# Kernel tuning notes

Measured on AMD Instinct MI355X. Metric: run time of the kernel, lower is better.

## Reference

```python
import jax, jax.numpy as jnp
import numpy as np

S = 2048          # sequence length (single prefill sequence)
HID = 4096        # hidden_size
NH, NKV, HD = 32, 8, 128   # q heads, kv heads, head_dim
THETA = 10000.0
SCALE = HD ** -0.5


def setup_inputs() -> dict:
    key = jax.random.key(0)
    k1, k2, k3 = jax.random.split(key, 3)
    hidden_states = jax.random.normal(k1, (S, HID), jnp.float32)
    positions = jnp.arange(S, dtype=jnp.int32)
    W_qkv = jax.random.normal(k2, (HID, (NH + 2 * NKV) * HD), jnp.float32) * 0.02
    W_o = jax.random.normal(k3, (NH * HD, HID), jnp.float32) * 0.02
    return {"hidden_states": hidden_states, "positions": positions,
            "W_qkv": W_qkv, "W_o": W_o}


def _rope(x, positions):
    # x: [T, H, HD]; neox-style RoPE (rotate halves, is_neox_style=True)
    half = HD // 2
    inv_freq = 1.0 / (THETA ** (jnp.arange(half, dtype=jnp.float32) / half))
    freqs = positions.astype(jnp.float32)[:, None] * inv_freq[None, :]  # [T, half]
    cos = jnp.cos(freqs)[:, None, :]
    sin = jnp.sin(freqs)[:, None, :]
    x1, x2 = x[..., :half], x[..., half:]
    return jnp.concatenate([x1 * cos - x2 * sin, x2 * cos + x1 * sin], axis=-1)


def reference(hidden_states, positions, W_qkv, W_o):
    # fused QKV projection then split (q_size = NH*HD, kv_size = NKV*HD)
    qkv = hidden_states @ W_qkv                      # [S, (NH+2*NKV)*HD]
    q, k, v = jnp.split(qkv, [NH * HD, NH * HD + NKV * HD], axis=1)
    q = _rope(q.reshape(S, NH, HD), positions)       # [S, NH, HD]
    k = _rope(k.reshape(S, NKV, HD), positions)      # [S, NKV, HD]
    v = v.reshape(S, NKV, HD)
    # GQA: broadcast kv heads to query heads
    rep = NH // NKV
    k = jnp.repeat(k, rep, axis=1)                   # [S, NH, HD]
    v = jnp.repeat(v, rep, axis=1)
    scores = jnp.einsum('qhd,khd->hqk', q, k) * SCALE  # [NH, S, S]
    causal = jnp.tril(jnp.ones((S, S), dtype=bool))
    scores = jnp.where(causal[None], scores, jnp.finfo(scores.dtype).min)
    attn = jax.nn.softmax(scores, axis=-1)
    out = jnp.einsum('hqk,khd->qhd', attn, v).reshape(S, NH * HD)
    return out @ W_o                                 # [S, HID]
```

## Files before the change

kernel.cpp:

```cpp
#include <hip/hip_runtime.h>
#include <math.h>
#include <stdint.h>

#define S_LEN 2048
#define HID 4096
#define NH 32
#define NKV 8
#define HD 128
#define QKV_N ((NH + 2*NKV) * HD)
#define NQK (NH + NKV)
static __device__ __constant__ const float SCALE_F = 0.08838834764831845f;

typedef __bf16 bf16x8 __attribute__((ext_vector_type(8)));
typedef __bf16 bf16x4 __attribute__((ext_vector_type(4)));
typedef float  f32x4  __attribute__((ext_vector_type(4)));
typedef uint32_t u32x4 __attribute__((ext_vector_type(4)));

#define GLD_LDS(gptr, lptr) \
  __builtin_amdgcn_global_load_lds( \
      (const __attribute__((address_space(1))) uint32_t*)(gptr), \
      (__attribute__((address_space(3))) uint32_t*)(lptr), 16, 0, 0)

__device__ __forceinline__ void tp64(const float* __restrict__ in, __bf16* __restrict__ out,
                                     int R, int C, int bx, int by, int tid, float* tile) {
  int lr = tid >> 4;
  int lc = (tid & 15) * 4;
  #pragma unroll
  for (int p = 0; p < 4; ++p) {
    int r = p * 16 + lr;
    const float4 v = *(const float4*)&in[(size_t)(by + r) * C + bx + lc];
    float* t = &tile[r * 65 + lc];
    t[0] = v.x; t[1] = v.y; t[2] = v.z; t[3] = v.w;
  }
  __syncthreads();
  int oc = tid >> 5;
  int orr = (tid & 31) * 2;
  #pragma unroll
  for (int p = 0; p < 8; ++p) {
    int c = p * 8 + oc;
    float v0 = tile[orr * 65 + c];
    float v1 = tile[(orr + 1) * 65 + c];
    __bf16 b2[2] = { (__bf16)v0, (__bf16)v1 };
    *(uint32_t*)&out[(size_t)(bx + c) * R + by + orr] = *(uint32_t*)b2;
  }
}

__global__ __launch_bounds__(256) void fused_prep_kernel(const float* __restrict__ hidden,
                                                         __bf16* __restrict__ hid_bf,
                                                         const float* __restrict__ Wqkv,
                                                         __bf16* __restrict__ wqkvT) {
  __shared__ float tile[64 * 65];
  const int b = blockIdx.x;
  const int tid = threadIdx.x;
  if (b < 2048) {
    const float4* in4 = (const float4*)hidden;
    int i = b * 256 + tid;
    #pragma unroll
    for (int k = 0; k < 4; ++k) {
      float4 v = in4[i + k * 524288];
      bf16x4 o = { (__bf16)v.x, (__bf16)v.y, (__bf16)v.z, (__bf16)v.w };
      *(bf16x4*)(hid_bf + (size_t)(i + k * 524288) * 4) = o;
    }
  } else {
    int id = b - 2048;
    int bx = (id % 96) * 64, by = (id / 96) * 64;
    tp64(Wqkv, wqkvT, HID, QKV_N, bx, by, tid, tile);
  }
}

__global__ __launch_bounds__(256) void fused_rope_tpv_kernel(const __bf16* __restrict__ qkv,
                                                             const int* __restrict__ pos,
                                                             __bf16* __restrict__ Qr,
                                                             __bf16* __restrict__ Kr,
                                                             __bf16* __restrict__ Vt) {
  __shared__ __bf16 tile[32][33];
  const int b = blockIdx.x;
  const int tid = threadIdx.x;
  if (b < 20480) {
    int idx = b * 256 + tid;
    int half = idx & 63;
    int t = idx >> 6;
    int hh = t % NQK;
    int s = t / NQK;
    if (s >= S_LEN) return;
    float p = (float)pos[s];
    float inv_freq = exp2f((float)half * -0.2076205059304601f);
    float ang = p * inv_freq;
    float cs = cosf(ang), sn = sinf(ang);
    const __bf16* src; __bf16* dst;
    if (hh < NH) {
      src = qkv + (size_t)s * QKV_N + (size_t)hh * HD;
      dst = Qr + ((size_t)s * NH + hh) * HD;
    } else {
      int kh = hh - NH;
      src = qkv + (size_t)s * QKV_N + (size_t)NH * HD + (size_t)kh * HD;
      dst = Kr + ((size_t)s * NKV + kh) * HD;
    }
    float x1 = (float)src[half], x2 = (float)src[half + 64];
    dst[half]      = (__bf16)(x1 * cs - x2 * sn);
    dst[half + 64] = (__bf16)(x2 * cs + x1 * sn);
  } else {
    int id = b - 20480;
    int sb = (id & 63) * 32;
    int db = ((id >> 6) & 3) * 32;
    int kvh = id >> 8;
    int tx = tid & 31, ty = tid >> 5;
    const __bf16* src = qkv + (size_t)(NH + NKV) * HD + (size_t)kvh * HD;
    for (int i = 0; i < 32; i += 8)
      tile[ty + i][tx] = src[(size_t)(sb + ty + i) * QKV_N + db + tx];
    __syncthreads();
    for (int i = 0; i < 32; i += 8)
      Vt[((size_t)kvh * HD + db + ty + i) * S_LEN + sb + tx] = tile[tx][ty + i];
  }
}

template <int BN, typename OutT>
__global__ __launch_bounds__(512, 2) void gemm_flat_kernel(const __bf16* __restrict__ A,
                                                           const __bf16* __restrict__ Bt,
                                                           OutT* __restrict__ C,
                                                           int M, int N, int K) {
  constexpr int NF = BN / 64;
  constexpr uint32_t ABUF = 8192u;
  constexpr uint32_t BBUF = (uint32_t)BN * 64u;
  __shared__ __align__(16) __bf16 sA[4 * 128 * 32];
  __shared__ __align__(16) __bf16 sB[4 * BN * 32];
  const int tid = threadIdx.x;
  const int lane = tid & 63;
  const int wave = tid >> 6;
  const int quad = lane >> 4;
  const int l16 = lane & 15;
  const int wm = (wave >> 2) * 64;
  const int wn = (wave & 3) * (BN / 4);

  const int nx = gridDim.x, ny = gridDim.y;
  const int nwg = nx * ny;
  int lin = blockIdx.y * nx + blockIdx.x;
  size_t bm, bn;
  if ((nwg & 7) == 0) {
    int swz = (lin & 7) * (nwg >> 3) + (lin >> 3);
    bm = (size_t)(swz % ny) * 128;
    bn = (size_t)(swz / ny) * BN;
  } else {
    bm = (size_t)blockIdx.y * 128;
    bn = (size_t)blockIdx.x * BN;
  }

  const int NT = K >> 5;
  const int rsw = (l16 >> 1) & 3;

  f32x4 acc[4][NF] = {};
  bf16x8 aR[2][4], bR[2][NF];

  const int rowA = tid >> 2;
  const int chL = (tid & 3) ^ ((tid >> 3) & 3);
  const uint64_t offB = (uint64_t)128 * K * 2;
  uint64_t aGA = (uint64_t)(uintptr_t)A + ((bm + rowA) * (size_t)K) * 2 + (size_t)chL * 16;
  uint64_t bGA = (uint64_t)(uintptr_t)Bt + ((bn + rowA) * (size_t)K) * 2 + (size_t)chL * 16;

  typedef __attribute__((address_space(3))) __bf16 lds_bf16;
  const uint32_t sAb = (uint32_t)(uintptr_t)(lds_bf16*)&sA[0];
  const uint32_t sBb = (uint32_t)(uintptr_t)(lds_bf16*)&sB[0];
  const uint32_t wlds = (uint32_t)__builtin_amdgcn_readfirstlane(wave * 1024);
  const uint32_t aBase = sAb + (uint32_t)(((wm + l16) * 32 + (quad ^ rsw) * 8) * 2);
  const uint32_t bBase = sBb + (uint32_t)(((wn + l16) * 32 + (quad ^ rsw) * 8) * 2);

#define STAGEA(ga, boff) \
  asm volatile("s_mov_b32 m0, %0\n\t" \
               "global_load_lds_dwordx4 %1, off" \
               :: "s"(sAb + (boff) + wlds), "v"(ga) : "memory")

#define STAGEB2(ga, boff) \
  asm volatile("s_mov_b32 m0, %0\n\t" \
               "global_load_lds_dwordx4 %2, off\n\t" \
               "s_mov_b32 m0, %1\n\t" \
               "global_load_lds_dwordx4 %3, off" \
               :: "s"(sBb + (boff) + wlds), "s"(sBb + (boff) + wlds + 8192u), \
                  "v"(ga), "v"((ga) + offB) : "memory")

#define STAGEB3(ga, boff) \
  asm volatile("s_mov_b32 m0, %0\n\t" \
               "global_load_lds_dwordx4 %3, off\n\t" \
               "s_mov_b32 m0, %1\n\t" \
               "global_load_lds_dwordx4 %4, off\n\t" \
               "s_mov_b32 m0, %2\n\t" \
               "global_load_lds_dwordx4 %5, off" \
               :: "s"(sBb + (boff) + wlds), "s"(sBb + (boff) + wlds + 8192u), \
                  "s"(sBb + (boff) + wlds + 16384u), \
                  "v"(ga), "v"((ga) + offB), "v"((ga) + 2 * offB) : "memory")

#define DSRD4(dst, baseaddr) do {                                                 \
    u32x4 t0_, t1_, t2_, t3_;                                                     \
    asm volatile("ds_read_b128 %0, %4\n\t"                                        \
                 "ds_read_b128 %1, %4 offset:1024\n\t"                            \
                 "ds_read_b128 %2, %4 offset:2048\n\t"                            \
                 "ds_read_b128 %3, %4 offset:3072"                                \
                 : "=&v"(t0_), "=&v"(t1_), "=&v"(t2_), "=&v"(t3_)                 \
                 : "v"(baseaddr));                                                \
    dst[0] = __builtin_bit_cast(bf16x8, t0_);                                     \
    dst[1] = __builtin_bit_cast(bf16x8, t1_);                                     \
    dst[2] = __builtin_bit_cast(bf16x8, t2_);                                     \
    dst[3] = __builtin_bit_cast(bf16x8, t3_);                                     \
  } while (0)

#define DSRD6(dst, baseaddr) do {                                                 \
    u32x4 t0_, t1_, t2_, t3_, t4_, t5_;                                           \
    asm volatile("ds_read_b128 %0, %6\n\t"                                        \
                 "ds_read_b128 %1, %6 offset:1024\n\t"                            \
                 "ds_read_b128 %2, %6 offset:2048\n\t"                            \
                 "ds_read_b128 %3, %6 offset:3072\n\t"                            \
                 "ds_read_b128 %4, %6 offset:4096\n\t"                            \
                 "ds_read_b128 %5, %6 offset:5120"                                \
                 : "=&v"(t0_), "=&v"(t1_), "=&v"(t2_), "=&v"(t3_),                \
                   "=&v"(t4_), "=&v"(t5_)                                         \
                 : "v"(baseaddr));                                                \
    dst[0] = __builtin_bit_cast(bf16x8, t0_);                                     \
    dst[1] = __builtin_bit_cast(bf16x8, t1_);                                     \
    dst[2] = __builtin_bit_cast(bf16x8, t2_);                                     \
    dst[3] = __builtin_bit_cast(bf16x8, t3_);                                     \
    dst[4] = __builtin_bit_cast(bf16x8, t4_);                                     \
    dst[5] = __builtin_bit_cast(bf16x8, t5_);                                     \
  } while (0)

#define BARX() __builtin_amdgcn_s_barrier()
#define SCB()  __builtin_amdgcn_sched_barrier(0)

  uint32_t nxtA = ABUF, nxtB = BBUF;
  uint32_t n3A = 3u * ABUF, n3B = 3u * BBUF;

  #pragma unroll
  for (int q = 0; q < 3; ++q) {
    STAGEA(aGA + q * 64, (uint32_t)q * ABUF);
    if constexpr (NF == 6) STAGEB3(bGA + q * 64, (uint32_t)q * BBUF);
    else                   STAGEB2(bGA + q * 64, (uint32_t)q * BBUF);
  }
  aGA += 192; bGA += 192;
  if constexpr (NF == 6) asm volatile("s_waitcnt vmcnt(8)");
  else                   asm volatile("s_waitcnt vmcnt(6)");
  SCB();
  BARX();
  DSRD4(aR[0], aBase);
  if constexpr (NF == 6) DSRD6(bR[0], bBase); else DSRD4(bR[0], bBase);

#define PHASE(P) do {                                                             \
    if constexpr (NF == 6) asm volatile("s_waitcnt vmcnt(4)");                    \
    else                   asm volatile("s_waitcnt vmcnt(3)");                    \
    SCB();                                                                        \
    BARX();                                                                       \
    DSRD4(aR[(P) ^ 1], aBase + nxtA);                                             \
    if constexpr (NF == 6) DSRD6(bR[(P) ^ 1], bBase + nxtB);                      \
    else                   DSRD4(bR[(P) ^ 1], bBase + nxtB);                      \
    STAGEA(aGA, n3A);                                                             \
    if constexpr (NF == 6) STAGEB3(bGA, n3B); else STAGEB2(bGA, n3B);             \
    aGA += 64; bGA += 64;                                                         \
    if constexpr (NF == 6) asm volatile("s_waitcnt lgkmcnt(10)");                 \
    else                   asm volatile("s_waitcnt lgkmcnt(8)");                  \
    SCB();                                                                        \
    __builtin_amdgcn_s_setprio(1);                                                \
    _Pragma("unroll")                                                             \
    for (int i_ = 0; i_ < 4; ++i_)                                                \
      _Pragma("unroll")                                                           \
      for (int j_ = 0; j_ < NF; ++j_)                                             \
        acc[i_][j_] = __builtin_amdgcn_mfma_f32_16x16x32_bf16(                    \
            aR[P][i_], bR[P][j_], acc[i_][j_], 0, 0, 0);                          \
    __builtin_amdgcn_s_setprio(0);                                                \
    SCB();                                                                        \
    nxtA = (nxtA == 3u * ABUF) ? 0u : nxtA + ABUF;                                \
    nxtB = (nxtB == 3u * BBUF) ? 0u : nxtB + BBUF;                                \
    n3A  = (n3A  == 3u * ABUF) ? 0u : n3A + ABUF;                                 \
    n3B  = (n3B  == 3u * BBUF) ? 0u : n3B + BBUF;                                 \
  } while (0)

  for (int u = 0; u < (NT >> 1); ++u) {
    PHASE(0);
    PHASE(1);
  }

  asm volatile("s_waitcnt vmcnt(0) lgkmcnt(0)");
  SCB();

  #pragma unroll
  for (int i = 0; i < 4; ++i)
    #pragma unroll
    for (int j = 0; j < NF; ++j)
      #pragma unroll
      for (int r = 0; r < 4; ++r) {
        size_t row = bm + wm + i * 16 + quad * 4 + r;
        size_t col = bn + wn + j * 16 + l16;
        C[row * (size_t)N + col] = (OutT)acc[i][j][r];
      }

#undef STAGEA
#undef STAGEB2
#undef STAGEB3
#undef DSRD4
#undef DSRD6
#undef BARX
#undef SCB
#undef PHASE
}

__global__ __launch_bounds__(256, 2) void attn_kernel(const __bf16* __restrict__ Qr,
                                                      const __bf16* __restrict__ Kr,
                                                      const __bf16* __restrict__ Vt,
                                                      __bf16* __restrict__ O,
                                                      const float* __restrict__ Wo,
                                                      __bf16* __restrict__ woT) {
  __shared__ __align__(16) char smem[73728];
  __bf16* Ps = (__bf16*)(smem + 65536);

  const int bid = blockIdx.x;
  const int tid = threadIdx.x;
  if (bid >= 512) {
    int id = bid - 512;
    int bx = (id & 63) * 64, by = (id >> 6) * 64;
    tp64(Wo, woT, HID, HID, bx, by, tid, (float*)smem);
    return;
  }

  const int h = bid & (NH - 1);
  const int j = bid >> 5;
  const int qb = (j < 8) ? (15 - j) : (j - 8);
  const int kvh = h >> 2;
  const int lane = tid & 63, wave = tid >> 6;
  const int quad = lane >> 4, l16 = lane & 15;
  const int sw = l16 & 7;
  const int q0 = qb * 128;

#define STAGE_KV(kbase, bufv) do {                                                 \
    char* kd_ = smem + (bufv) * 16384;                                             \
    char* vd_ = smem + 32768 + (bufv) * 16384;                                     \
    _Pragma("unroll")                                                              \
    for (int pass_ = 0; pass_ < 4; ++pass_) {                                      \
      int c_ = pass_ * 256 + tid;                                                  \
      int row_ = c_ >> 4, ch_ = c_ & 15;                                           \
      int chs_ = ch_ ^ (row_ & 7);                                                 \
      GLD_LDS(&Kr[(size_t)((kbase) + row_) * (NKV * HD) + (size_t)kvh * HD + chs_ * 8], \
              kd_ + c_ * 16);                                                      \
    }                                                                              \
    _Pragma("unroll")                                                              \
    for (int pass_ = 0; pass_ < 4; ++pass_) {                                      \
      int c_ = pass_ * 256 + tid;                                                  \
      int d_ = c_ >> 3, ch_ = c_ & 7;                                              \
      int chs_ = ch_ ^ (d_ & 7);                                                   \
      GLD_LDS(&Vt[((size_t)kvh * HD + d_) * S_LEN + (kbase) + chs_ * 8],           \
              vd_ + c_ * 16);                                                      \
    }                                                                              \
  } while (0)

#define SOFTMAX_SET(scX, m2X, liX, oaccX, maskCond, pfX) do {                      \
    float s_[16];                                                                  \
    _Pragma("unroll")                                                              \
    for (int jt_ = 0; jt_ < 4; ++jt_)                                              \
      _Pragma("unroll")                                                            \
      for (int r_ = 0; r_ < 4; ++r_) s_[jt_ * 4 + r_] = scX[jt_][r_];              \
    if (maskCond) {                                                                \
      int qloc_ = wave * 16 + l16;                                                 \
      _Pragma("unroll")                                                            \
      for (int jt_ = 0; jt_ < 4; ++jt_)                                            \
        _Pragma("unroll")                                                          \
        for (int r_ = 0; r_ < 4; ++r_)                                             \
          if (jt_ * 16 + quad * 4 + r_ > qloc_) s_[jt_ * 4 + r_] = -INFINITY;      \
    }                                                                              \
    float mx_ = s_[0];                                                             \
    _Pragma("unroll")                                                              \
    for (int i_ = 1; i_ < 16; ++i_) mx_ = fmaxf(mx_, s_[i_]);                      \
    mx_ = fmaxf(mx_, __shfl_xor(mx_, 16, 64));                                     \
    mx_ = fmaxf(mx_, __shfl_xor(mx_, 32, 64));                                     \
    float mxs_ = mx_ * C2;                                                         \
    if (!__all(mxs_ <= m2X + 11.54f)) {                                            \
      float m2n_ = fmaxf(m2X, mxs_);                                               \
      float al_ = exp2f(m2X - m2n_);                                               \
      liX *= al_;                                                                  \
      _Pragma("unroll")                                                            \
      for (int dt_ = 0; dt_ < 8; ++dt_) oaccX[dt_] *= al_;                         \
      m2X = m2n_;                                                                  \
    }                                                                              \
    float sum_ = 0.0f;                                                             \
    __bf16* pw_ = Ps + wave * 1024 + l16 * 64;                                     \
    _Pragma("unroll")                                                              \
    for (int jt_ = 0; jt_ < 4; ++jt_) {                                            \
      float e0_ = exp2f(fmaf(s_[jt_*4+0], C2, -m2X));                              \
      float e1_ = exp2f(fmaf(s_[jt_*4+1], C2, -m2X));                              \
      float e2_ = exp2f(fmaf(s_[jt_*4+2], C2, -m2X));                              \
      float e3_ = exp2f(fmaf(s_[jt_*4+3], C2, -m2X));                              \
      sum_ += (e0_ + e1_) + (e2_ + e3_);                                           \
      bf16x4 pk_ = { (__bf16)e0_, (__bf16)e1_, (__bf16)e2_, (__bf16)e3_ };         \
      int ch_ = jt_ * 2 + (quad >> 1);                                             \
      *(bf16x4*)&pw_[((ch_ ^ sw) * 8) + (quad & 1) * 4] = pk_;                     \
    }                                                                              \
    sum_ += __shfl_xor(sum_, 16, 64);                                              \
    sum_ += __shfl_xor(sum_, 32, 64);                                              \
    liX += sum_;                                                                   \
    pfX[0] = *(const bf16x8*)&pw_[((quad) ^ sw) * 8];                              \
    pfX[1] = *(const bf16x8*)&pw_[((4 + quad) ^ sw) * 8];                          \
  } while (0)

  bf16x8 qf[2][4];
  #pragma unroll
  for (int s2 = 0; s2 < 2; ++s2) {
    const __bf16* qp = Qr + (size_t)(q0 + s2 * 64 + wave * 16 + l16) * (NH * HD)
                          + (size_t)h * HD + quad * 8;
    #pragma unroll
    for (int kk = 0; kk < 4; ++kk) qf[s2][kk] = *(const bf16x8*)(qp + kk * 32);
  }
  f32x4 oacc[2][8] = {};
  float m2[2] = { -INFINITY, -INFINITY }, l_i[2] = { 0.0f, 0.0f };
  const float C2 = SCALE_F * 1.4426950408889634f;
  bf16x8 pf0[2], pf1[2];

  int buf = 0;
  STAGE_KV(0, 0);
  for (int kb = 0; kb <= q0; kb += 64) {
    __syncthreads();
    STAGE_KV(kb + 64, buf ^ 1);

    const __bf16* Ks = (const __bf16*)(smem + buf * 16384);
    const __bf16* Vs = (const __bf16*)(smem + 32768 + buf * 16384);

    f32x4 sc0[4] = {}, sc1[4] = {};
    __builtin_amdgcn_s_setprio(1);
    for (int jt = 0; jt < 4; ++jt)
      for (int kk = 0; kk < 4; ++kk) {
        bf16x8 kf = *(const bf16x8*)&Ks[(jt * 16 + l16) * 128 + ((kk * 4 + quad) ^ sw) * 8];
        sc0[jt] = __builtin_amdgcn_mfma_f32_16x16x32_bf16(kf, qf[0][kk], sc0[jt], 0, 0, 0);
        sc1[jt] = __builtin_amdgcn_mfma_f32_16x16x32_bf16(kf, qf[1][kk], sc1[jt], 0, 0, 0);
      }
    __builtin_amdgcn_s_setprio(0);

    SOFTMAX_SET(sc0, m2[0], l_i[0], oacc[0], (kb == q0), pf0);
    SOFTMAX_SET(sc1, m2[1], l_i[1], oacc[1], false, pf1);

    __builtin_amdgcn_s_setprio(1);
    for (int half = 0; half < 2; ++half)
      for (int dt = 0; dt < 8; ++dt) {
        bf16x8 vf = *(const bf16x8*)&Vs[(dt * 16 + l16) * 64 + ((half * 4 + quad) ^ sw) * 8];
        oacc[0][dt] = __builtin_amdgcn_mfma_f32_16x16x32_bf16(vf, pf0[half], oacc[0][dt], 0, 0, 0);
        oacc[1][dt] = __builtin_amdgcn_mfma_f32_16x16x32_bf16(vf, pf1[half], oacc[1][dt], 0, 0, 0);
      }
    __builtin_amdgcn_s_setprio(0);
    buf ^= 1;
  }
  {
    __syncthreads();
    const __bf16* Ks = (const __bf16*)(smem + buf * 16384);
    const __bf16* Vs = (const __bf16*)(smem + 32768 + buf * 16384);

    f32x4 sc1[4] = {};
    __builtin_amdgcn_s_setprio(1);
    for (int jt = 0; jt < 4; ++jt)
      for (int kk = 0; kk < 4; ++kk) {
        bf16x8 kf = *(const bf16x8*)&Ks[(jt * 16 + l16) * 128 + ((kk * 4 + quad) ^ sw) * 8];
        sc1[jt] = __builtin_amdgcn_mfma_f32_16x16x32_bf16(kf, qf[1][kk], sc1[jt], 0, 0, 0);
      }
    __builtin_amdgcn_s_setprio(0);

    SOFTMAX_SET(sc1, m2[1], l_i[1], oacc[1], true, pf1);

    __builtin_amdgcn_s_setprio(1);
    for (int half = 0; half < 2; ++half)
      for (int dt = 0; dt < 8; ++dt) {
        bf16x8 vf = *(const bf16x8*)&Vs[(dt * 16 + l16) * 64 + ((half * 4 + quad) ^ sw) * 8];
        oacc[1][dt] = __builtin_amdgcn_mfma_f32_16x16x32_bf16(vf, pf1[half], oacc[1][dt], 0, 0, 0);
      }
    __builtin_amdgcn_s_setprio(0);
  }
  __syncthreads();

#undef STAGE_KV
#undef SOFTMAX_SET

  float* scr = (float*)smem + wave * 2112;
  #pragma unroll
  for (int s2 = 0; s2 < 2; ++s2) {
    float inv = 1.0f / l_i[s2];
    #pragma unroll
    for (int dt = 0; dt < 8; ++dt) {
      f32x4 v = oacc[s2][dt] * inv;
      *(f32x4*)&scr[l16 * 132 + dt * 16 + quad * 4] = v;
    }
    #pragma unroll
    for (int it = 0; it < 4; ++it) {
      int c = it * 64 + lane;
      int row = c >> 4, ch = c & 15;
      const float* sp = &scr[row * 132 + ch * 8];
      f32x4 a = *(const f32x4*)sp;
      f32x4 b = *(const f32x4*)(sp + 4);
      bf16x8 o = { (__bf16)a[0], (__bf16)a[1], (__bf16)a[2], (__bf16)a[3],
                   (__bf16)b[0], (__bf16)b[1], (__bf16)b[2], (__bf16)b[3] };
      *(bf16x8*)&O[(size_t)(q0 + s2 * 64 + wave * 16 + row) * (NH * HD)
                   + (size_t)h * HD + ch * 8] = o;
    }
  }
}

extern "C" void kernel_launch(void* const* d_in, const int* in_sizes, int n_in,
                              void* d_out, int out_size, void* d_ws, size_t ws_size,
                              hipStream_t stream) {
  const float* hidden    = (const float*)d_in[0];
  const int*   positions = (const int*)d_in[1];
  const float* Wqkv      = (const float*)d_in[2];
  const float* Wo        = (const float*)d_in[3];
  float* out = (float*)d_out;

  char* p = (char*)d_ws;
  auto alloc = [&](size_t bytes) { char* r = p; p += (bytes + 255) & ~(size_t)255; return r; };
  __bf16* hid_bf = (__bf16*)alloc((size_t)S_LEN * HID * 2);
  __bf16* wqkvT  = (__bf16*)alloc((size_t)QKV_N * HID * 2);
  __bf16* qkv    = (__bf16*)alloc((size_t)S_LEN * QKV_N * 2);
  __bf16* Qr     = (__bf16*)alloc((size_t)S_LEN * NH * HD * 2);
  __bf16* Kr     = (__bf16*)alloc((size_t)S_LEN * NKV * HD * 2);
  __bf16* Vt     = (__bf16*)alloc((size_t)S_LEN * NKV * HD * 2);
  __bf16* attn   = hid_bf;
  __bf16* woT    = wqkvT;

  fused_prep_kernel<<<8192, 256, 0, stream>>>(hidden, hid_bf, Wqkv, wqkvT);
  gemm_flat_kernel<384, __bf16><<<dim3(QKV_N / 384, S_LEN / 128, 1), 512, 0, stream>>>(
      hid_bf, wqkvT, qkv, S_LEN, QKV_N, HID);
  fused_rope_tpv_kernel<<<22528, 256, 0, stream>>>(qkv, positions, Qr, Kr, Vt);
  attn_kernel<<<512 + 4096, 256, 0, stream>>>(Qr, Kr, Vt, attn, Wo, woT);
  gemm_flat_kernel<256, float><<<dim3(HID / 256, S_LEN / 128, 1), 512, 0, stream>>>(
      attn, woT, out, S_LEN, HID, HID);
}
```

Baseline: 460.1 us.

## Add triple-buffered 128x256 GEMM kernel for output projection

Adds a new GEMM kernel using a 128x256 tile and a three-stage LDS ring, where data is loaded directly from global memory into LDS through inline-asm global_load_lds. It also uses swizzled LDS reads, explicit waitcnt/barrier scheduling, setprio around MFMA blocks, and a grouped workgroup swizzle for cache locality. The output projection GEMM now uses this kernel instead of the generic flat GEMM, aiming to overlap loads with MFMA better. The hand-scheduled asm waits carry a correctness risk if the vmcnt accounting is wrong.

```diff
diff --git a/kernel.cpp b/kernel.cpp
--- a/kernel.cpp
+++ b/kernel.cpp
@@ -297,6 +297,156 @@
 #undef BARX
 #undef SCB
 #undef PHASE
+}
+
+template <typename OutT>
+__global__ __launch_bounds__(512, 2) void gemm128_kernel(const __bf16* __restrict__ A,
+                                                         const __bf16* __restrict__ Bt,
+                                                         OutT* __restrict__ C,
+                                                         int M, int N, int K) {
+  __shared__ __align__(16) __bf16 sA[3][2][128 * 32];
+  __shared__ __align__(16) __bf16 sB[3][2][256 * 32];
+  const int tid = threadIdx.x;
+  const int lane = tid & 63;
+  const int wave = tid >> 6;
+  const int quad = lane >> 4;
+  const int l16 = lane & 15;
+  const int wm = (wave >> 2) * 64;
+  const int wn = (wave & 3) * 64;
+
+  const int nx = gridDim.x, ny = gridDim.y;
+  const int nwg = nx * ny;
+  int lin = blockIdx.y * nx + blockIdx.x;
+  size_t bm, bn;
+  if ((nwg & 7) == 0) {
+    int swz = (lin & 7) * (nwg >> 3) + (lin >> 3);
+    bm = (size_t)(swz % ny) * 128;
+    bn = (size_t)(swz / ny) * 256;
+  } else {
+    bm = (size_t)blockIdx.y * 128;
+    bn = (size_t)blockIdx.x * 256;
+  }
+
+  const int NT = K >> 6;
+  const int rsw = (l16 >> 1) & 3;
+
+  f32x4 acc[4][4] = {};
+  bf16x8 aR[4], bR[4];
+
+  const int rowA = tid >> 2;
+  const int chLs = (tid & 3) ^ ((tid >> 3) & 3);
+  const uint64_t off128B = (uint64_t)128 * K * 2;
+  uint64_t aGA = (uint64_t)(uintptr_t)A + ((bm + rowA) * (size_t)K) * 2 + (size_t)chLs * 16;
+  uint64_t bGA = (uint64_t)(uintptr_t)Bt + ((bn + rowA) * (size_t)K) * 2 + (size_t)chLs * 16;
+
+  typedef __attribute__((address_space(3))) __bf16 lds_bf16;
+  const uint32_t sAb = (uint32_t)(uintptr_t)(lds_bf16*)&sA[0][0][0];
+  const uint32_t sBb = (uint32_t)(uintptr_t)(lds_bf16*)&sB[0][0][0];
+  const uint32_t wlds = (uint32_t)__builtin_amdgcn_readfirstlane(wave * 1024);
+  const uint32_t aBase = sAb + (uint32_t)(((wm + l16) * 32 + (quad ^ rsw) * 8) * 2);
+  const uint32_t bBase = sBb + (uint32_t)(((wn + l16) * 32 + (quad ^ rsw) * 8) * 2);
+
+#define STA128(ga, ldsoff) \
+  asm volatile("s_mov_b32 m0, %0\n\t" \
+               "global_load_lds_dwordx4 %1, off" \
+               :: "s"((ldsoff) + wlds), "v"(ga) : "memory")
+
+#define STB128(ga, ldsoff) \
+  asm volatile("s_mov_b32 m0, %0\n\t" \
+               "global_load_lds_dwordx4 %2, off\n\t" \
+               "s_mov_b32 m0, %1\n\t" \
+               "global_load_lds_dwordx4 %3, off" \
+               :: "s"((ldsoff) + wlds), "s"((ldsoff) + wlds + 8192u), \
+                  "v"(ga), "v"((ga) + off128B) : "memory")
+
+#define DSRD4(dst, baseaddr) do {                                                 \
+    u32x4 t0_, t1_, t2_, t3_;                                                     \
+    asm volatile("ds_read_b128 %0, %4\n\t"                                        \
+                 "ds_read_b128 %1, %4 offset:1024\n\t"                            \
+                 "ds_read_b128 %2, %4 offset:2048\n\t"                            \
+                 "ds_read_b128 %3, %4 offset:3072"                                \
+                 : "=&v"(t0_), "=&v"(t1_), "=&v"(t2_), "=&v"(t3_)                 \
+                 : "v"(baseaddr));                                                \
+    dst[0] = __builtin_bit_cast(bf16x8, t0_);                                     \
+    dst[1] = __builtin_bit_cast(bf16x8, t1_);                                     \
+    dst[2] = __builtin_bit_cast(bf16x8, t2_);                                     \
+    dst[3] = __builtin_bit_cast(bf16x8, t3_);                                     \
+  } while (0)
+
+#define IS_A(aoff, kh) DSRD4(aR, aBase + (aoff) + (kh) * 8192u)
+#define IS_B(boff, kh) DSRD4(bR, bBase + (boff) + (kh) * 16384u)
+
+#define MFMA16Q() do {                                                            \
+    __builtin_amdgcn_s_setprio(1);                                                \
+    _Pragma("unroll")                                                             \
+    for (int i_ = 0; i_ < 4; ++i_)                                                \
+      _Pragma("unroll")                                                           \
+      for (int j_ = 0; j_ < 4; ++j_)                                              \
+        acc[i_][j_] = __builtin_amdgcn_mfma_f32_16x16x32_bf16(                    \
+            aR[i_], bR[j_], acc[i_][j_], 0, 0, 0);                                \
+    __builtin_amdgcn_s_setprio(0);                                                \
+    __builtin_amdgcn_sched_barrier(0);                                            \
+  } while (0)
+
+#define BARX() __builtin_amdgcn_s_barrier()
+#define LGKM0X() do { asm volatile("s_waitcnt lgkmcnt(0)");                       \
+                      __builtin_amdgcn_sched_barrier(0); } while (0)
+#define VMCNT6X() do { asm volatile("s_waitcnt vmcnt(6)");                        \
+                       __builtin_amdgcn_sched_barrier(0); } while (0)
+
+  uint32_t curA = 0u, nxtA = 16384u, stgA = 32768u;
+  uint32_t curB = 0u, nxtB = 32768u, stgB = 65536u;
+
+  STA128(aGA,       sAb + 0u);
+  STA128(aGA + 64,  sAb + 8192u);
+  STB128(bGA,       sBb + 0u);
+  STB128(bGA + 64,  sBb + 16384u);
+  STA128(aGA + 128, sAb + 16384u);
+  STA128(aGA + 192, sAb + 16384u + 8192u);
+  STB128(bGA + 128, sBb + 32768u);
+  STB128(bGA + 192, sBb + 32768u + 16384u);
+  aGA += 256; bGA += 256;
+  VMCNT6X();
+  BARX();
+
+  for (int t = 0; t < NT; ++t) {
+    IS_A(curA, 0); IS_B(curB, 0);
+    STA128(aGA, sAb + stgA);
+    STB128(bGA, sBb + stgB);
+    BARX(); LGKM0X(); MFMA16Q(); BARX();
+    IS_A(curA, 1); IS_B(curB, 1);
+    STA128(aGA + 64, sAb + stgA + 8192u);
+    STB128(bGA + 64, sBb + stgB + 16384u);
+    aGA += 128; bGA += 128;
+    VMCNT6X();
+    BARX(); LGKM0X(); MFMA16Q(); BARX();
+    uint32_t ta = curA; curA = nxtA; nxtA = stgA; stgA = ta;
+    uint32_t tb = curB; curB = nxtB; nxtB = stgB; stgB = tb;
+  }
+
+  asm volatile("s_waitcnt vmcnt(0) lgkmcnt(0)");
+  __builtin_amdgcn_sched_barrier(0);
+
+  #pragma unroll
+  for (int i = 0; i < 4; ++i)
+    #pragma unroll
+    for (int j = 0; j < 4; ++j)
+      #pragma unroll
+      for (int r = 0; r < 4; ++r) {
+        size_t row = bm + wm + i * 16 + quad * 4 + r;
+        size_t col = bn + wn + j * 16 + l16;
+        C[row * (size_t)N + col] = (OutT)acc[i][j][r];
+      }
+
+#undef STA128
+#undef STB128
+#undef DSRD4
+#undef IS_A
+#undef IS_B
+#undef MFMA16Q
+#undef BARX
+#undef LGKM0X
+#undef VMCNT6X
 }
 
 __global__ __launch_bounds__(256, 2) void attn_kernel(const __bf16* __restrict__ Qr,
@@ -518,6 +668,6 @@
       hid_bf, wqkvT, qkv, S_LEN, QKV_N, HID);
   fused_rope_tpv_kernel<<<22528, 256, 0, stream>>>(qkv, positions, Qr, Kr, Vt);
   attn_kernel<<<512 + 4096, 256, 0, stream>>>(Qr, Kr, Vt, attn, Wo, woT);
-  gemm_flat_kernel<256, float><<<dim3(HID / 256, S_LEN / 128, 1), 512, 0, stream>>>(
+  gemm128_kernel<float><<<dim3(HID / 256, S_LEN / 128, 1), 512, 0, stream>>>(
       attn, woT, out, S_LEN, HID, HID);
 }
```

Result: no change. 458.2 us (-0.4%).
